# Optimization experiments

Measured on AMD Instinct MI355X. Metric: run time of the kernel, lower is better.

Reference implementation:

```python
import jax, jax.numpy as jnp
import numpy as np

B, NT, NC, NN = 2, 64, 1024, 1024
C, H = 1024, 16
HD = C // H
N = NT + NC + NN
EPS = 1e-5
NEG = -1e30


def _ln(t, w, b):
    # LayerNorm over last dim (head_dim), torch eps=1e-5
    mu = jnp.mean(t, axis=-1, keepdims=True)
    var = jnp.mean(jnp.square(t - mu), axis=-1, keepdims=True)
    return (t - mu) * jax.lax.rsqrt(var + EPS) * w + b


def _rope(q, k, pos):
    # q,k: [B,H,S,HD]; pos: [B,S]; rotate-half RoPE, base 10000
    hd = q.shape[-1]
    half = hd // 2
    inv_freq = 1.0 / (10000.0 ** (jnp.arange(half, dtype=jnp.float32) / half))
    ang = pos.astype(jnp.float32)[:, None, :, None] * inv_freq  # [B,1,S,half]
    cos, sin = jnp.cos(ang), jnp.sin(ang)
    def rot(t):
        t1, t2 = t[..., :half], t[..., half:]
        return jnp.concatenate([t1 * cos - t2 * sin, t2 * cos + t1 * sin], axis=-1)
    return rot(q), rot(k)


def setup_inputs() -> dict:
    key = jax.random.key(0)
    ks = jax.random.split(key, 4)
    s = 0.02
    return {
        "x": jax.random.normal(ks[0], (B, N, C), jnp.float32),
        "position_ids": jnp.broadcast_to(jnp.arange(NC + NN, dtype=jnp.int32), (B, NC + NN)),
        "text_position_ids": jnp.broadcast_to(jnp.arange(NT, dtype=jnp.int32), (B, NT)),
        "attention_mask": jnp.tril(jnp.ones((N, N), dtype=bool)),
        "n_text": NT, "n_clean": NC, "n_noised": NN,
        "qkv_w": jax.random.normal(ks[1], (3, 3 * C, C), jnp.float32) * s,
        "qkv_b": jnp.zeros((3, 3 * C), jnp.float32),
        "qn_w": jnp.ones((3, HD), jnp.float32),
        "qn_b": jnp.zeros((3, HD), jnp.float32),
        "kn_w": jnp.ones((3, HD), jnp.float32),
        "kn_b": jnp.zeros((3, HD), jnp.float32),
        "proj_w": jax.random.normal(ks[2], (3, C, C), jnp.float32) * s,
        "proj_b": jnp.zeros((3, C), jnp.float32),
    }


def reference(x, position_ids, text_position_ids, attention_mask, n_text, n_clean, n_noised,
              qkv_w, qkv_b, qn_w, qn_b, kn_w, kn_b, proj_w, proj_b):
    Bx, Nx, Cx = x.shape
    hd = qn_w.shape[-1]
    nh = Cx // hd
    b0, b1 = n_text, n_text + n_clean
    segs = (x[:, :b0], x[:, b0:b1], x[:, b1:])  # text / clean / noised

    qs, kks, vvs = [], [], []
    for i, xs in enumerate(segs):
        S = xs.shape[1]
        qkv = jnp.einsum('bsc,oc->bso', xs, qkv_w[i]) + qkv_b[i]
        qkv = qkv.reshape(Bx, S, 3, nh, hd).transpose(2, 0, 3, 1, 4)  # [3,B,H,S,hd]
        q = _ln(qkv[0], qn_w[i], qn_b[i])
        k = _ln(qkv[1], kn_w[i], kn_b[i])
        qs.append(q); kks.append(k); vvs.append(qkv[2])

    img_q = jnp.concatenate([qs[1], qs[2]], axis=2)
    img_k = jnp.concatenate([kks[1], kks[2]], axis=2)
    img_q, img_k = _rope(img_q, img_k, position_ids)
    txt_q, txt_k = _rope(qs[0], kks[0], text_position_ids)

    q = jnp.concatenate([txt_q, img_q], axis=2)
    k = jnp.concatenate([txt_k, img_k], axis=2)
    v = jnp.concatenate(vvs, axis=2)

    scale = 1.0 / np.sqrt(hd).astype(np.float32)
    scores = jnp.einsum('bhqd,bhkd->bhqk', q, k) * scale
    scores = jnp.where(attention_mask, scores, NEG)
    attn = jax.nn.softmax(scores, axis=-1)
    out = jnp.einsum('bhqk,bhkd->bhqd', attn, v)
    out = out.transpose(0, 2, 1, 3).reshape(Bx, Nx, Cx)

    o_segs = (out[:, :b0], out[:, b0:b1], out[:, b1:])
    outs = [jnp.einsum('bsc,oc->bso', o_segs[i], proj_w[i]) + proj_b[i] for i in range(3)]
    return jnp.concatenate(outs, axis=1)
```

## Files before the change

### kernel.cpp

```cpp
#include <hip/hip_runtime.h>
#include <hip/hip_bf16.h>

#define BB   2
#define NT   64
#define NC   1024
#define NN   1024
#define NTOK (NT + NC + NN)
#define CC   1024
#define HH   16
#define HD   64
#define K3   (3 * CC)
#define EPSV 1e-5f

typedef __attribute__((ext_vector_type(8))) short short8;
typedef __attribute__((ext_vector_type(4))) float f32x4;
typedef __attribute__((ext_vector_type(4))) float float4v;

__device__ __forceinline__ short bf16raw(float x) {
    __hip_bfloat16 h = __float2bfloat16(x);
    return *(short*)&h;
}

#define GL_LDS(gptr, lptr) \
    __builtin_amdgcn_global_load_lds( \
        (const __attribute__((address_space(1))) void*)(gptr), \
        (__attribute__((address_space(3))) void*)(lptr), 16, 0, 0)

__constant__ signed char QB_tab[33] =
    {16,16,16,15,15,15,14,14,14,13,13,13,12,12,12,11,11,10,10,9,9,8,8,7,7,6,6,5,4,3,2,1,0};
__constant__ signed char CH_tab[33] =
    { 0, 1, 2, 0, 1, 2, 0, 1, 2, 0, 1, 2, 0, 1, 2, 0, 1, 0, 1,0,1,0,1,0,1,0,1,0,0,0,0,0,0};

__global__ __launch_bounds__(256) void cast_all(
    const float* __restrict__ s0, const float* __restrict__ s1, const float* __restrict__ s2,
    __hip_bfloat16* __restrict__ d0, __hip_bfloat16* __restrict__ d1, __hip_bfloat16* __restrict__ d2,
    int n0, int n1, int n2)
{
    int i = blockIdx.x * 256 + threadIdx.x;
    int stride = gridDim.x * 256;
    int ntot = n0 + n1 + n2;
    for (; i < ntot; i += stride) {
        const float* sp; short* dp; int j;
        if (i < n0)            { sp = s0; dp = (short*)d0; j = i; }
        else if (i < n0 + n1)  { sp = s1; dp = (short*)d1; j = i - n0; }
        else                   { sp = s2; dp = (short*)d2; j = i - n0 - n1; }
        float4v v = *(const float4v*)(sp + (size_t)j * 4);
        short4 o;
        o.x = bf16raw(v.x); o.y = bf16raw(v.y); o.z = bf16raw(v.z); o.w = bf16raw(v.w);
        *(short4*)(dp + (size_t)j * 4) = o;
    }
}

__global__ __launch_bounds__(256) void gemm_qkv(
    const __hip_bfloat16* __restrict__ A,
    const __hip_bfloat16* __restrict__ Wb,
    const float* __restrict__ biasb,
    const float* __restrict__ qn_w, const float* __restrict__ qn_b,
    const float* __restrict__ kn_w, const float* __restrict__ kn_b,
    __hip_bfloat16* __restrict__ Q,
    __hip_bfloat16* __restrict__ Kg,
    __hip_bfloat16* __restrict__ Vt)
{
    __shared__ short lds[32768];
    short* buf = lds;

    int tid = threadIdx.x;
    int lane = tid & 63, w = tid >> 6;
    int l15 = lane & 15, quad = lane >> 4;
    int wm = w >> 1, wn = w & 1;
    int r7 = l15 & 7;

    int y = blockIdx.y;
    int seg, tm;
    if (y < 16)      { seg = 1; tm = y * 128; }
    else if (y < 32) { seg = 2; tm = (y - 16) * 128; }
    else             { seg = 0; tm = 0; }
    int S = (seg == 0) ? 64 : 1024;
    int seg_start = (seg == 0) ? 0 : (seg == 1 ? NT : NT + NC);
    const short* W = (const short*)Wb + (size_t)seg * K3 * CC;
    const float* bias = biasb + (size_t)seg * K3;
    int tileN = blockIdx.x * 128;

    const short* aptr[4];
    const short* bptr[4];
#pragma unroll
    for (int j = 0; j < 4; ++j) {
        int c = j * 256 + tid;
        int row = c >> 3, u = (c & 7) ^ (row & 7);
        int ar = tm + row;
        int arow = (ar / S) * NTOK + seg_start + (ar % S);
        aptr[j] = (const short*)A + (size_t)arow * CC + u * 8;
        bptr[j] = W + (size_t)(tileN + row) * CC + u * 8;
    }

    f32x4 zero = {0.f, 0.f, 0.f, 0.f};
    f32x4 acc[4][4];
#pragma unroll
    for (int mb = 0; mb < 4; ++mb)
#pragma unroll
        for (int nb = 0; nb < 4; ++nb) acc[mb][nb] = zero;

#pragma unroll
    for (int j = 0; j < 4; ++j) {
        int c8 = (j * 256 + tid) * 8;
        GL_LDS(aptr[j], lds + c8);
        GL_LDS(bptr[j], lds + 8192 + c8);
    }
    __syncthreads();

    int cur = 0;
    for (int k0 = 64; k0 <= CC; k0 += 64) {
        short* As = lds + cur * 16384;
        short* Bs = As + 8192;
        if (k0 < CC) {
            short* An = lds + (cur ^ 1) * 16384;
#pragma unroll
            for (int j = 0; j < 4; ++j) {
                int c8 = (j * 256 + tid) * 8;
                GL_LDS(aptr[j] + k0, An + c8);
                GL_LDS(bptr[j] + k0, An + 8192 + c8);
            }
        }

#pragma unroll
        for (int s = 0; s < 2; ++s) {
            int sx = ((s * 4 + quad) ^ r7) * 8;
            short8 af[4], bf[4];
#pragma unroll
            for (int mb = 0; mb < 4; ++mb)
                af[mb] = *(const short8*)&As[(wm * 64 + mb * 16 + l15) * 64 + sx];
#pragma unroll
            for (int nb = 0; nb < 4; ++nb)
                bf[nb] = *(const short8*)&Bs[(wn * 64 + nb * 16 + l15) * 64 + sx];
#pragma unroll
            for (int mb = 0; mb < 4; ++mb)
#pragma unroll
                for (int nb = 0; nb < 4; ++nb)
                    acc[mb][nb] = __builtin_amdgcn_mfma_f32_16x16x32_bf16(af[mb], bf[nb], acc[mb][nb], 0, 0, 0);
        }
        __syncthreads();
        cur ^= 1;
    }

    int sect = tileN >> 10;

    if (sect < 2) {
        const float* nw = (sect == 0 ? qn_w : kn_w) + seg * HD;
        const float* nbv = (sect == 0 ? qn_b : kn_b) + seg * HD;
        float lw[4], lb[4], bcol[4];
#pragma unroll
        for (int nb = 0; nb < 4; ++nb) {
            lw[nb] = nw[nb * 16 + l15];
            lb[nb] = nbv[nb * 16 + l15];
            bcol[nb] = bias[tileN + wn * 64 + nb * 16 + l15];
        }
        float qscale = (sect == 0) ? 0.18033688011112042f : 1.0f;

        float invf0 = expf(-9.210340371976184f * (float)l15 * (1.0f / 32.0f));
        float invf1 = expf(-9.210340371976184f * (float)(16 + l15) * (1.0f / 32.0f));
        float cd0, sd0, cd1, sd1;
        sincosf(invf0, &sd0, &cd0);
        sincosf(invf1, &sd1, &cd1);

#pragma unroll
        for (int mb = 0; mb < 4; ++mb) {
            int tok0 = wm * 64 + mb * 16 + quad * 4;
            int ar0 = tm + tok0;
            int nloc0 = ar0 % S;
            int pos0 = (seg == 0) ? nloc0 : (seg_start + nloc0 - NT);
            float c0, s0, c1, s1v;
            sincosf((float)pos0 * invf0, &s0, &c0);
            sincosf((float)pos0 * invf1, &s1v, &c1);

#pragma unroll
            for (int r = 0; r < 4; ++r) {
                int tok = tok0 + r;
                float v[4];
#pragma unroll
                for (int nb = 0; nb < 4; ++nb) v[nb] = acc[mb][nb][r] + bcol[nb];

                float t1 = v[0] + v[1] + v[2] + v[3];
                float t2 = v[0] * v[0] + v[1] * v[1] + v[2] * v[2] + v[3] * v[3];
#pragma unroll
                for (int off = 8; off >= 1; off >>= 1) {
                    t1 += __shfl_xor(t1, off);
                    t2 += __shfl_xor(t2, off);
                }
                float mu = t1 * (1.0f / 64.0f);
                float var = t2 * (1.0f / 64.0f) - mu * mu;
                float rstd = rsqrtf(var + EPSV);
#pragma unroll
                for (int nb = 0; nb < 4; ++nb) v[nb] = (v[nb] - mu) * rstd * lw[nb] + lb[nb];

                short* bp = &buf[tok * 134 + wn * 64];
                bp[0 * 16 + l15] = bf16raw((v[0] * c0 - v[2] * s0) * qscale);
                bp[1 * 16 + l15] = bf16raw((v[1] * c1 - v[3] * s1v) * qscale);
                bp[2 * 16 + l15] = bf16raw((v[2] * c0 + v[0] * s0) * qscale);
                bp[3 * 16 + l15] = bf16raw((v[3] * c1 + v[1] * s1v) * qscale);

                float nc0 = c0 * cd0 - s0 * sd0, ns0 = s0 * cd0 + c0 * sd0;
                float nc1 = c1 * cd1 - s1v * sd1, ns1 = s1v * cd1 + c1 * sd1;
                c0 = nc0; s0 = ns0; c1 = nc1; s1v = ns1;
            }
        }
        __syncthreads();
        __hip_bfloat16* dst = (sect == 0) ? Q : Kg;
        int head_base = (tileN & 1023) >> 6;
#pragma unroll
        for (int it = 0; it < 8; ++it) {
            int idx = it * 256 + tid;
            int tok = idx >> 4, cc = (idx & 15) * 8;
            int ar = tm + tok;
            int bb = ar / S;
            int nloc = seg_start + (ar % S);
            int hh2 = head_base + (cc >> 6), d = cc & 63;
            *(short8*)((short*)dst + ((size_t)(bb * HH + hh2) * NTOK + nloc) * HD + d) =
                *(const short8*)&buf[tok * 134 + cc];
        }
    } else {
        float bcol[4];
#pragma unroll
        for (int nb = 0; nb < 4; ++nb) bcol[nb] = bias[tileN + wn * 64 + nb * 16 + l15];
#pragma unroll
        for (int mb = 0; mb < 4; ++mb) {
#pragma unroll
            for (int r = 0; r < 4; ++r) {
                int tok = wm * 64 + mb * 16 + quad * 4 + r;
#pragma unroll
                for (int nb = 0; nb < 4; ++nb) {
                    int col = wn * 64 + nb * 16 + l15;
                    buf[col * 134 + tok] = bf16raw(acc[mb][nb][r] + bcol[nb]);
                }
            }
        }
        __syncthreads();
#pragma unroll
        for (int it = 0; it < 8; ++it) {
            int idx = it * 256 + tid;
            int row = idx >> 4;
            int tc = (idx & 15) * 8;
            int vcol = (tileN - 2048) + row;
            int h = vcol >> 6, d = vcol & 63;
            int ar = tm + tc;
            int bb = ar / S;
            int nloc = seg_start + (ar % S);
            short8 val = *(const short8*)&buf[row * 134 + tc];
            *(short8*)((short*)Vt + ((size_t)(bb * HH + h) * HD + d) * NTOK + nloc) = val;
        }
    }
}

__global__ __launch_bounds__(256) void gemm_proj(
    const __hip_bfloat16* __restrict__ A,
    const __hip_bfloat16* __restrict__ Wb,
    const float* __restrict__ biasb,
    float* __restrict__ Cout)
{
    __shared__ short lds[24576];

    int tid = threadIdx.x;
    int lane = tid & 63, w = tid >> 6;
    int l15 = lane & 15, quad = lane >> 4;
    int wm = w >> 1, wn = w & 1;
    int r7 = l15 & 7;

    int y = blockIdx.y;
    int seg, tm;
    if (y < 32)      { seg = 1; tm = y * 64; }
    else if (y < 64) { seg = 2; tm = (y - 32) * 64; }
    else             { seg = 0; tm = (y - 64) * 64; }
    int S = (seg == 0) ? 64 : 1024;
    int seg_start = (seg == 0) ? 0 : (seg == 1 ? NT : NT + NC);
    const short* W = (const short*)Wb + (size_t)seg * CC * CC;
    const float* bias = biasb + (size_t)seg * CC;
    int tileN = blockIdx.x * 128;

    const short* aptr[2];
    const short* bptr[4];
#pragma unroll
    for (int j = 0; j < 2; ++j) {
        int c = j * 256 + tid;
        int row = c >> 3, u = (c & 7) ^ (row & 7);
        int ar = tm + row;
        int arow = (ar / S) * NTOK + seg_start + (ar % S);
        aptr[j] = (const short*)A + (size_t)arow * CC + u * 8;
    }
#pragma unroll
    for (int j = 0; j < 4; ++j) {
        int c = j * 256 + tid;
        int row = c >> 3, u = (c & 7) ^ (row & 7);
        bptr[j] = W + (size_t)(tileN + row) * CC + u * 8;
    }

    f32x4 zero = {0.f, 0.f, 0.f, 0.f};
    f32x4 acc[2][4];
#pragma unroll
    for (int mb = 0; mb < 2; ++mb)
#pragma unroll
        for (int nb = 0; nb < 4; ++nb) acc[mb][nb] = zero;

#pragma unroll
    for (int j = 0; j < 2; ++j)
        GL_LDS(aptr[j], lds + (j * 256 + tid) * 8);
#pragma unroll
    for (int j = 0; j < 4; ++j)
        GL_LDS(bptr[j], lds + 4096 + (j * 256 + tid) * 8);
    __syncthreads();

    int cur = 0;
    for (int k0 = 64; k0 <= CC; k0 += 64) {
        short* As = lds + cur * 12288;
        short* Bs = As + 4096;
        if (k0 < CC) {
            short* An = lds + (cur ^ 1) * 12288;
#pragma unroll
            for (int j = 0; j < 2; ++j)
                GL_LDS(aptr[j] + k0, An + (j * 256 + tid) * 8);
#pragma unroll
            for (int j = 0; j < 4; ++j)
                GL_LDS(bptr[j] + k0, An + 4096 + (j * 256 + tid) * 8);
        }

#pragma unroll
        for (int s = 0; s < 2; ++s) {
            int sx = ((s * 4 + quad) ^ r7) * 8;
            short8 af[2], bf[4];
#pragma unroll
            for (int mb = 0; mb < 2; ++mb)
                af[mb] = *(const short8*)&As[(wm * 32 + mb * 16 + l15) * 64 + sx];
#pragma unroll
            for (int nb = 0; nb < 4; ++nb)
                bf[nb] = *(const short8*)&Bs[(wn * 64 + nb * 16 + l15) * 64 + sx];
#pragma unroll
            for (int mb = 0; mb < 2; ++mb)
#pragma unroll
                for (int nb = 0; nb < 4; ++nb)
                    acc[mb][nb] = __builtin_amdgcn_mfma_f32_16x16x32_bf16(af[mb], bf[nb], acc[mb][nb], 0, 0, 0);
        }
        __syncthreads();
        cur ^= 1;
    }

#pragma unroll
    for (int mb = 0; mb < 2; ++mb) {
#pragma unroll
        for (int r = 0; r < 4; ++r) {
            int ar = tm + wm * 32 + mb * 16 + quad * 4 + r;
            int crow = (ar / S) * NTOK + seg_start + (ar % S);
            float* cp = Cout + (size_t)crow * CC + tileN;
#pragma unroll
            for (int nb = 0; nb < 4; ++nb) {
                int col = wn * 64 + nb * 16 + l15;
                cp[col] = acc[mb][nb][r] + bias[tileN + col];
            }
        }
    }
}

__global__ __launch_bounds__(512) void attn_part(
    const __hip_bfloat16* __restrict__ Q,
    const __hip_bfloat16* __restrict__ Kg,
    const __hip_bfloat16* __restrict__ Vt,
    __hip_bfloat16* __restrict__ O,
    float* __restrict__ Opart,
    float* __restrict__ lpart)
{
    __shared__ short Ks[2][4096];
    __shared__ short Vs[2][4096];
    __shared__ short Ps[8][16 * 72];

    int tid = threadIdx.x;
    int lane = tid & 63, w = tid >> 6;
    int quad = lane >> 4, l15 = lane & 15;
    int r7 = l15 & 7;
    int bh = blockIdx.y, b = bh >> 4, h = bh & 15;

    int e = blockIdx.x;
    int qb = QB_tab[e], c = CH_tab[e];
    int q0 = qb * 128;
    int nt = 2 * qb + 2; if (nt > 33) nt = 33;
    int t0 = c * 12, t1 = t0 + 12; if (t1 > nt) t1 = nt;
    bool direct = (nt <= 12);

    size_t base = (size_t)bh * NTOK * HD;

    int qrow = q0 + w * 16 + l15;
    int qr_c = qrow < NTOK ? qrow : NTOK - 1;
    short8 qf0 = *(const short8*)((const short*)Q + base + (size_t)qr_c * HD + quad * 8);
    short8 qf1 = *(const short8*)((const short*)Q + base + (size_t)qr_c * HD + 32 + quad * 8);

    int srow = tid >> 3;
    int su = (tid & 7) ^ (srow & 7);
    const short* kptr = (const short*)Kg + base + (size_t)srow * HD + su * 8;
    const short* vptr = (const short*)Vt + base + (size_t)srow * NTOK + su * 8;
    int c8 = tid * 8;

    f32x4 zero = {0.f, 0.f, 0.f, 0.f};
    f32x4 oacc[4] = {zero, zero, zero, zero};
    float l[4] = {0.f, 0.f, 0.f, 0.f};

    int qmin_w = q0 + w * 16;
    int qmax_w = qmin_w + 15;
    int sx0 = (quad ^ r7) * 8;
    int sx1 = ((4 + quad) ^ r7) * 8;

    GL_LDS(kptr + (size_t)(t0 * 64) * HD, Ks[0] + c8);
    GL_LDS(vptr + t0 * 64, Vs[0] + c8);
    __syncthreads();

    int cur = 0;
    for (int t = t0; t < t1; ++t) {
        if (t + 1 < t1) {
            GL_LDS(kptr + (size_t)((t + 1) * 64) * HD, Ks[cur ^ 1] + c8);
            GL_LDS(vptr + (t + 1) * 64, Vs[cur ^ 1] + c8);
        }

        if (t * 64 <= qmax_w) {
            f32x4 s[4];
            __builtin_amdgcn_s_setprio(1);
#pragma unroll
            for (int kb = 0; kb < 4; ++kb) {
                int krow = (kb * 16 + l15) * 64;
                short8 kf0 = *(const short8*)&Ks[cur][krow + sx0];
                short8 kf1 = *(const short8*)&Ks[cur][krow + sx1];
                f32x4 z = zero;
                z = __builtin_amdgcn_mfma_f32_16x16x32_bf16(qf0, kf0, z, 0, 0, 0);
                z = __builtin_amdgcn_mfma_f32_16x16x32_bf16(qf1, kf1, z, 0, 0, 0);
                s[kb] = z;
            }
            __builtin_amdgcn_s_setprio(0);

            if (t * 64 + 63 <= qmin_w) {
#pragma unroll
                for (int r = 0; r < 4; ++r)
#pragma unroll
                    for (int kb = 0; kb < 4; ++kb) {
                        float p = __builtin_amdgcn_exp2f(s[kb][r]);
                        Ps[w][(quad * 4 + r) * 72 + kb * 16 + l15] = bf16raw(p);
                        l[r] += p;
                    }
            } else {
#pragma unroll
                for (int r = 0; r < 4; ++r) {
                    int qg = q0 + w * 16 + quad * 4 + r;
#pragma unroll
                    for (int kb = 0; kb < 4; ++kb) {
                        int kgk = t * 64 + kb * 16 + l15;
                        float p = (kgk <= qg) ? __builtin_amdgcn_exp2f(s[kb][r]) : 0.f;
                        Ps[w][(quad * 4 + r) * 72 + kb * 16 + l15] = bf16raw(p);
                        l[r] += p;
                    }
                }
            }

            __builtin_amdgcn_wave_barrier();

            __builtin_amdgcn_s_setprio(1);
#pragma unroll
            for (int sl = 0; sl < 2; ++sl) {
                short8 pf = *(const short8*)&Ps[w][l15 * 72 + sl * 32 + quad * 8];
                int vsx = ((sl * 4 + quad) ^ r7) * 8;
#pragma unroll
                for (int db = 0; db < 4; ++db) {
                    short8 vf = *(const short8*)&Vs[cur][(db * 16 + l15) * 64 + vsx];
                    oacc[db] = __builtin_amdgcn_mfma_f32_16x16x32_bf16(pf, vf, oacc[db], 0, 0, 0);
                }
            }
            __builtin_amdgcn_s_setprio(0);
        }

        __syncthreads();
        cur ^= 1;
    }

#pragma unroll
    for (int r = 0; r < 4; ++r) {
#pragma unroll
        for (int off = 8; off >= 1; off >>= 1) l[r] += __shfl_xor(l[r], off);
    }

    if (direct) {
#pragma unroll
        for (int r = 0; r < 4; ++r) {
            int qg = q0 + w * 16 + quad * 4 + r;
            float inv_l = 1.0f / l[r];
#pragma unroll
            for (int db = 0; db < 4; ++db) {
                O[(size_t)(b * NTOK + qg) * CC + h * HD + db * 16 + l15] =
                    __float2bfloat16(oacc[db][r] * inv_l);
            }
        }
    } else {
        int pidx = (bh * 17 + qb) * 3 + c;
        float* op = Opart + (size_t)pidx * (128 * 64);
#pragma unroll
        for (int r = 0; r < 4; ++r) {
            int q = w * 16 + quad * 4 + r;
#pragma unroll
            for (int db = 0; db < 4; ++db)
                op[q * 64 + db * 16 + l15] = oacc[db][r];
            if (l15 == 0) lpart[pidx * 128 + q] = l[r];
        }
    }
}

__global__ __launch_bounds__(512) void attn_comb(
    const float* __restrict__ Opart, const float* __restrict__ lpart,
    __hip_bfloat16* __restrict__ O)
{
    __shared__ float ls[128];
    int tid = threadIdx.x;
    int qb = 6 + blockIdx.x;
    int bh = blockIdx.y, b = bh >> 4, h = bh & 15;
    int nt = 2 * qb + 2; if (nt > 33) nt = 33;
    int nch = (nt + 11) / 12;
    int q0 = qb * 128;
    int pbase = (bh * 17 + qb) * 3;

    if (tid < 128) {
        float s = 0.f;
        for (int cc = 0; cc < nch; ++cc) s += lpart[(pbase + cc) * 128 + tid];
        ls[tid] = 1.0f / s;
    }
    __syncthreads();

#pragma unroll
    for (int k = 0; k < 16; ++k) {
        int elem = k * 512 + tid;
        int q = elem >> 6, d = elem & 63;
        int qg = q0 + q;
        if (qg >= NTOK) continue;
        float s = 0.f;
        for (int cc = 0; cc < nch; ++cc)
            s += Opart[(size_t)(pbase + cc) * (128 * 64) + elem];
        O[(size_t)(b * NTOK + qg) * CC + h * HD + d] = __float2bfloat16(s * ls[q]);
    }
}

extern "C" void kernel_launch(void* const* d_in, const int* in_sizes, int n_in,
                              void* d_out, int out_size, void* d_ws, size_t ws_size,
                              hipStream_t stream) {
    const float* x      = (const float*)d_in[0];
    const float* qkv_w  = (const float*)d_in[7];
    const float* qkv_b  = (const float*)d_in[8];
    const float* qn_w   = (const float*)d_in[9];
    const float* qn_b   = (const float*)d_in[10];
    const float* kn_w   = (const float*)d_in[11];
    const float* kn_b   = (const float*)d_in[12];
    const float* proj_w = (const float*)d_in[13];
    const float* proj_b = (const float*)d_in[14];
    float* out = (float*)d_out;

    const size_t n_x    = (size_t)BB * NTOK * CC;
    const size_t n_qkvw = (size_t)3 * K3 * CC;
    const size_t n_prjw = (size_t)3 * CC * CC;
    const size_t n_part = (size_t)32 * 17 * 3;

    __hip_bfloat16* x_bf    = (__hip_bfloat16*)d_ws;
    __hip_bfloat16* qkvw_bf = x_bf + n_x;
    __hip_bfloat16* prjw_bf = qkvw_bf + n_qkvw;
    __hip_bfloat16* Qbf  = prjw_bf + n_prjw;
    __hip_bfloat16* Kbf  = Qbf + n_x;
    __hip_bfloat16* Vtbf = Kbf + n_x;
    float* Opart = (float*)(Vtbf + n_x);
    float* lpart = Opart + n_part * (128 * 64);
    __hip_bfloat16* attn_bf = x_bf;

    cast_all<<<1024, 256, 0, stream>>>(x, qkv_w, proj_w, x_bf, qkvw_bf, prjw_bf,
                                       (int)(n_x / 4), (int)(n_qkvw / 4), (int)(n_prjw / 4));

    gemm_qkv<<<dim3(K3 / 128, 33), 256, 0, stream>>>(
        x_bf, qkvw_bf, qkv_b,
        qn_w, qn_b, kn_w, kn_b, Qbf, Kbf, Vtbf);

    attn_part<<<dim3(33, BB * HH), 512, 0, stream>>>(Qbf, Kbf, Vtbf, attn_bf, Opart, lpart);

    attn_comb<<<dim3(11, BB * HH), 512, 0, stream>>>(Opart, lpart, attn_bf);

    gemm_proj<<<dim3(CC / 128, 66), 256, 0, stream>>>(attn_bf, prjw_bf, proj_b, out);
}
```

Before: 263.1 us.

## Use partial vmcnt waits so next-tile prefetch stays in flight during compute

The GEMM and attention loops swap __syncthreads (which drains every outstanding global-to-LDS load, including the just-issued prefetch) for explicit s_waitcnt vmcnt(N) plus raw s_barrier. Each loop now waits only for the current tile's loads, so the next tile's loads overlap the MFMA work. This depends on the vmcnt counts matching the exact number of issued loads, and on compiler memory fences being placed correctly. Any compiler-inserted extra loads could break correctness.

After: 270.4 us. 1.03x slower.

```diff
diff --git a/kernel.cpp b/kernel.cpp
--- a/kernel.cpp
+++ b/kernel.cpp
@@ -25,6 +25,12 @@
     __builtin_amdgcn_global_load_lds( \
         (const __attribute__((address_space(1))) void*)(gptr), \
         (__attribute__((address_space(3))) void*)(lptr), 16, 0, 0)
+
+#define WAIT_VM(N) asm volatile("s_waitcnt vmcnt(" #N ")" ::: "memory")
+#define BARRIER_FENCED() do { __builtin_amdgcn_s_barrier(); \
+                              asm volatile("" ::: "memory"); } while (0)
+#define FENCE_BARRIER()  do { asm volatile("" ::: "memory"); \
+                              __builtin_amdgcn_s_barrier(); } while (0)
 
 __constant__ signed char QB_tab[33] =
     {16,16,16,15,15,15,14,14,14,13,13,13,12,12,12,11,11,10,10,9,9,8,8,7,7,6,6,5,4,3,2,1,0};
@@ -108,19 +114,23 @@
     }
     __syncthreads();
 
-    int cur = 0;
-    for (int k0 = 64; k0 <= CC; k0 += 64) {
-        short* As = lds + cur * 16384;
+    for (int t = 0; t < 16; ++t) {
+        short* As = lds + (t & 1) * 16384;
         short* Bs = As + 8192;
-        if (k0 < CC) {
-            short* An = lds + (cur ^ 1) * 16384;
+        if (t < 15) {
+            short* An = lds + ((t + 1) & 1) * 16384;
+            int k0 = (t + 1) * 64;
 #pragma unroll
             for (int j = 0; j < 4; ++j) {
                 int c8 = (j * 256 + tid) * 8;
                 GL_LDS(aptr[j] + k0, An + c8);
                 GL_LDS(bptr[j] + k0, An + 8192 + c8);
             }
-        }
+            WAIT_VM(8);
+        } else {
+            WAIT_VM(0);
+        }
+        BARRIER_FENCED();
 
 #pragma unroll
         for (int s = 0; s < 2; ++s) {
@@ -138,8 +148,7 @@
                 for (int nb = 0; nb < 4; ++nb)
                     acc[mb][nb] = __builtin_amdgcn_mfma_f32_16x16x32_bf16(af[mb], bf[nb], acc[mb][nb], 0, 0, 0);
         }
-        __syncthreads();
-        cur ^= 1;
+        FENCE_BARRIER();
     }
 
     int sect = tileN >> 10;
@@ -307,19 +316,23 @@
         GL_LDS(bptr[j], lds + 4096 + (j * 256 + tid) * 8);
     __syncthreads();
 
-    int cur = 0;
-    for (int k0 = 64; k0 <= CC; k0 += 64) {
-        short* As = lds + cur * 12288;
+    for (int t = 0; t < 16; ++t) {
+        short* As = lds + (t & 1) * 12288;
         short* Bs = As + 4096;
-        if (k0 < CC) {
-            short* An = lds + (cur ^ 1) * 12288;
+        if (t < 15) {
+            short* An = lds + ((t + 1) & 1) * 12288;
+            int k0 = (t + 1) * 64;
 #pragma unroll
             for (int j = 0; j < 2; ++j)
                 GL_LDS(aptr[j] + k0, An + (j * 256 + tid) * 8);
 #pragma unroll
             for (int j = 0; j < 4; ++j)
                 GL_LDS(bptr[j] + k0, An + 4096 + (j * 256 + tid) * 8);
-        }
+            WAIT_VM(6);
+        } else {
+            WAIT_VM(0);
+        }
+        BARRIER_FENCED();
 
 #pragma unroll
         for (int s = 0; s < 2; ++s) {
@@ -337,8 +350,7 @@
                 for (int nb = 0; nb < 4; ++nb)
                     acc[mb][nb] = __builtin_amdgcn_mfma_f32_16x16x32_bf16(af[mb], bf[nb], acc[mb][nb], 0, 0, 0);
         }
-        __syncthreads();
-        cur ^= 1;
+        FENCE_BARRIER();
     }
 
 #pragma unroll
@@ -413,7 +425,11 @@
         if (t + 1 < t1) {
             GL_LDS(kptr + (size_t)((t + 1) * 64) * HD, Ks[cur ^ 1] + c8);
             GL_LDS(vptr + (t + 1) * 64, Vs[cur ^ 1] + c8);
-        }
+            WAIT_VM(2);
+        } else {
+            WAIT_VM(0);
+        }
+        BARRIER_FENCED();
 
         if (t * 64 <= qmax_w) {
             f32x4 s[4];
@@ -469,7 +485,7 @@
             __builtin_amdgcn_s_setprio(0);
         }
 
-        __syncthreads();
+        FENCE_BARRIER();
         cur ^= 1;
     }
 
```

## Swizzle GEMM block order across XCDs and overlap prefetch with fine-grained waits

Applied to the files above, without the earlier changes.

Both GEMM kernels remap the linear block id so that consecutive blocks, which are dispatched round-robin across the 8 XCDs, land on nearby tiles. This is meant to improve L2 reuse of the A and W tiles. The QKV GEMM main loop also replaces __syncthreads with an explicit vmcnt wait plus raw barriers. The next tile's global-to-LDS loads can then stay in flight while the current tile is computed. The hand-counted vmcnt and the grid dimensions (24x33, 8x66) are assumed by the code, so a shape change would break correctness.

Measured after the change: 264.9 us. Within noise of the previous version (+0.7%).

```diff
diff --git a/kernel.cpp b/kernel.cpp
--- a/kernel.cpp
+++ b/kernel.cpp
@@ -25,6 +25,12 @@
     __builtin_amdgcn_global_load_lds( \
         (const __attribute__((address_space(1))) void*)(gptr), \
         (__attribute__((address_space(3))) void*)(lptr), 16, 0, 0)
+
+#define WAIT_VM(N) asm volatile("s_waitcnt vmcnt(" #N ")" ::: "memory")
+#define BARRIER_FENCED() do { __builtin_amdgcn_s_barrier(); \
+                              asm volatile("" ::: "memory"); } while (0)
+#define FENCE_BARRIER()  do { asm volatile("" ::: "memory"); \
+                              __builtin_amdgcn_s_barrier(); } while (0)
 
 __constant__ signed char QB_tab[33] =
     {16,16,16,15,15,15,14,14,14,13,13,13,12,12,12,11,11,10,10,9,9,8,8,7,7,6,6,5,4,3,2,1,0};
@@ -70,7 +76,11 @@
     int wm = w >> 1, wn = w & 1;
     int r7 = l15 & 7;
 
-    int y = blockIdx.y;
+    int bid = blockIdx.y * 24 + blockIdx.x;
+    int swz = (bid & 7) * 99 + (bid >> 3);
+    int bx = swz % 24;
+    int y  = swz / 24;
+
     int seg, tm;
     if (y < 16)      { seg = 1; tm = y * 128; }
     else if (y < 32) { seg = 2; tm = (y - 16) * 128; }
@@ -79,7 +89,7 @@
     int seg_start = (seg == 0) ? 0 : (seg == 1 ? NT : NT + NC);
     const short* W = (const short*)Wb + (size_t)seg * K3 * CC;
     const float* bias = biasb + (size_t)seg * K3;
-    int tileN = blockIdx.x * 128;
+    int tileN = bx * 128;
 
     const short* aptr[4];
     const short* bptr[4];
@@ -108,19 +118,23 @@
     }
     __syncthreads();
 
-    int cur = 0;
-    for (int k0 = 64; k0 <= CC; k0 += 64) {
-        short* As = lds + cur * 16384;
+    for (int t = 0; t < 16; ++t) {
+        short* As = lds + (t & 1) * 16384;
         short* Bs = As + 8192;
-        if (k0 < CC) {
-            short* An = lds + (cur ^ 1) * 16384;
+        if (t < 15) {
+            short* An = lds + ((t + 1) & 1) * 16384;
+            int k0 = (t + 1) * 64;
 #pragma unroll
             for (int j = 0; j < 4; ++j) {
                 int c8 = (j * 256 + tid) * 8;
                 GL_LDS(aptr[j] + k0, An + c8);
                 GL_LDS(bptr[j] + k0, An + 8192 + c8);
             }
-        }
+            WAIT_VM(8);
+        } else {
+            WAIT_VM(0);
+        }
+        BARRIER_FENCED();
 
 #pragma unroll
         for (int s = 0; s < 2; ++s) {
@@ -138,8 +152,7 @@
                 for (int nb = 0; nb < 4; ++nb)
                     acc[mb][nb] = __builtin_amdgcn_mfma_f32_16x16x32_bf16(af[mb], bf[nb], acc[mb][nb], 0, 0, 0);
         }
-        __syncthreads();
-        cur ^= 1;
+        FENCE_BARRIER();
     }
 
     int sect = tileN >> 10;
@@ -264,7 +277,11 @@
     int wm = w >> 1, wn = w & 1;
     int r7 = l15 & 7;
 
-    int y = blockIdx.y;
+    int bid = blockIdx.y * 8 + blockIdx.x;
+    int swz = (bid & 7) * 66 + (bid >> 3);
+    int bx = swz % 8;
+    int y  = swz / 8;
+
     int seg, tm;
     if (y < 32)      { seg = 1; tm = y * 64; }
     else if (y < 64) { seg = 2; tm = (y - 32) * 64; }
@@ -273,7 +290,7 @@
     int seg_start = (seg == 0) ? 0 : (seg == 1 ? NT : NT + NC);
     const short* W = (const short*)Wb + (size_t)seg * CC * CC;
     const float* bias = biasb + (size_t)seg * CC;
-    int tileN = blockIdx.x * 128;
+    int tileN = bx * 128;
 
     const short* aptr[2];
     const short* bptr[4];
```
